# Kernel optimization log

Hardware: AMD Instinct MI355X
Metric: run time of the kernel (lower is better)

The kernel has to match this reference:

```python
import jax, jax.numpy as jnp
import numpy as np

N_NODES = 100000
N_EDGES = 1600000
FEAT = 128
HIDDEN = 128
NUM_CLASSES = 40


def setup_inputs() -> dict:
    key = jax.random.key(0)
    ks = jax.random.split(key, 6)
    x = jax.random.normal(ks[0], (N_NODES, FEAT), dtype=jnp.float32)
    edge_index = jax.random.randint(ks[1], (2, N_EDGES), 0, N_NODES, dtype=jnp.int64)
    # GCNConv layer-1 params (glorot-ish scale) and trailing Linear params
    W1 = jax.random.normal(ks[2], (FEAT, HIDDEN), dtype=jnp.float32) / np.sqrt(FEAT)
    b1 = jnp.zeros((HIDDEN,), dtype=jnp.float32)
    lin_W = jax.random.normal(ks[3], (HIDDEN, NUM_CLASSES), dtype=jnp.float32) / np.sqrt(HIDDEN)
    lin_b = jnp.zeros((NUM_CLASSES,), dtype=jnp.float32)
    return {"x": x, "edge_index": edge_index, "W1": W1, "b1": b1,
            "lin_W": lin_W, "lin_b": lin_b}


def _gcn_conv(x, edge_index, W, b):
    """PyG GCNConv: out = D^{-1/2}(A+I)D^{-1/2} (x W) + b."""
    n = x.shape[0]
    self_loops = jnp.arange(n, dtype=edge_index.dtype)
    row = jnp.concatenate([edge_index[0], self_loops])  # source nodes
    col = jnp.concatenate([edge_index[1], self_loops])  # destination nodes
    deg = jax.ops.segment_sum(jnp.ones_like(col, dtype=x.dtype), col, num_segments=n)
    deg_inv_sqrt = jnp.where(deg > 0, jax.lax.rsqrt(deg), 0.0)
    norm = deg_inv_sqrt[row] * deg_inv_sqrt[col]  # [E+N]
    h = x @ W                                      # [N, H]
    msg = norm[:, None] * h[row]                   # [E+N, H] gather
    out = jax.ops.segment_sum(msg, col, num_segments=n)  # scatter-add
    return out + b


def reference(x, edge_index, W1, b1, lin_W, lin_b):
    h = _gcn_conv(x, edge_index, W1, b1)
    h = jax.nn.relu(h)
    # F.dropout with training=False (eval) is the identity
    logits = h @ lin_W + lin_b
    return jax.nn.log_softmax(logits, axis=1)
```

## Files before the change

### kernel.cpp

```cpp
#include <hip/hip_runtime.h>
#include <hip/hip_fp16.h>
#include <math.h>

#define N_NODES 100000
#define N_EDGES 1600000
#define NBUCK   1563
#define NBUCK_P 1568
#define NB_HIST 256
#define NB_BIN  256
#define DCAP    1536

#define OFF_BTOT   0x1000u
#define OFF_HS     0x780000u
#define OFF_WT     0x2100000u
#define OFF_WLT    0x2110000u
#define OFF_GHIST  0x3980000u
#define OFF_GCHOFF 0x3B10000u
#define OFF_DUMP   0x3CA0000u

typedef _Float16 half8_t __attribute__((ext_vector_type(8)));
typedef float f32x2_t __attribute__((ext_vector_type(2)));
typedef float f32x4_t __attribute__((ext_vector_type(4)));
typedef float f32x16_t __attribute__((ext_vector_type(16)));

__global__ __launch_bounds__(256) void k_hist(const int* __restrict__ p32,
                                              int* __restrict__ G_hist,
                                              const float* __restrict__ W,
                                              __half* __restrict__ Wt,
                                              const float* __restrict__ linW,
                                              __half* __restrict__ WlT) {
  const int t = threadIdx.x;
  if (blockIdx.x == NB_HIST + 16) {
    __shared__ float buf[5120];
#pragma unroll
    for (int i = 0; i < 5; ++i) {
      int lin = i * 256 + t;
      ((float4*)buf)[lin] = ((const float4*)linW)[lin];
    }
    __syncthreads();
#pragma unroll
    for (int i = 0; i < 4; ++i) {
      int lin = i * 256 + t;
      int c = lin >> 4, kb = lin & 15;
      union { __half h[8]; int4 v; } u;
#pragma unroll
      for (int q = 0; q < 8; ++q)
        u.h[q] = (c < 40) ? __float2half(buf[(kb * 8 + q) * 40 + c])
                          : __float2half(0.f);
      *(int4*)&WlT[(size_t)c * 128 + kb * 8] = u.v;
    }
    return;
  }
  if (blockIdx.x >= NB_HIST) {
    __shared__ float buf1[1024];
    const int b = blockIdx.x - NB_HIST;
    float4 v = ((const float4*)(W + (size_t)b * 1024))[t];
    *(float4*)&buf1[t * 4] = v;
    __syncthreads();
    if (t < 128) {
      union { __half h[8]; int4 v; } u;
#pragma unroll
      for (int k = 0; k < 8; ++k) u.h[k] = __float2half(buf1[k * 128 + t]);
      *(int4*)&Wt[(size_t)t * 128 + b * 8] = u.v;
    }
    return;
  }
  __shared__ int hist[NBUCK];
  __shared__ int nz;
  if (t == 0) nz = 0;
  for (int i = t; i < NBUCK; i += 256) hist[i] = 0;
  __syncthreads();
  if (p32[2 * t + 1] != 0) atomicAdd(&nz, 1);
  __syncthreads();
  const int s = (nz == 0) ? 1 : 0;
  const int base = blockIdx.x * 6250;
  for (int i = 0; i < 25; ++i) {
    int e = base + i * 256 + t;
    if (e < base + 6250) {
      int c = p32[((size_t)(N_EDGES + e)) << s];
      atomicAdd(&hist[c >> 6], 1);
    }
  }
  __syncthreads();
  for (int i = t; i < NBUCK; i += 256) G_hist[blockIdx.x * NBUCK_P + i] = hist[i];
}

__global__ __launch_bounds__(256) void k_bucket_scan(const int* __restrict__ G_hist,
                                                     int* __restrict__ G_choff,
                                                     int* __restrict__ btot) {
  __shared__ int wsum[4];
  const int t = threadIdx.x;
  const int b = blockIdx.x;
  const int c = G_hist[t * NBUCK_P + b];
  int sv = c;
  const int lane = t & 63;
  for (int d = 1; d < 64; d <<= 1) {
    int a = __shfl_up(sv, d);
    if (lane >= d) sv += a;
  }
  if (lane == 63) wsum[t >> 6] = sv;
  __syncthreads();
  int o = 0;
  for (int w2 = 0; w2 < (t >> 6); ++w2) o += wsum[w2];
  G_choff[t * NBUCK_P + b] = o + sv - c;
  if (t == 255) btot[b] = o + sv;
}

__global__ __launch_bounds__(512) void k_bin(const int* __restrict__ p32,
                                             const int* __restrict__ G_choff,
                                             int* __restrict__ dump) {
  __shared__ int gb[NBUCK];
  __shared__ int cur[NBUCK];
  __shared__ int nz;
  const int t = threadIdx.x;
  const int blk = blockIdx.x;
  if (t == 0) nz = 0;
  for (int i = t; i < NBUCK; i += 512) {
    gb[i] = i * DCAP + G_choff[blk * NBUCK_P + i];
    cur[i] = 0;
  }
  __syncthreads();
  if (t < 256 && p32[2 * t + 1] != 0) atomicAdd(&nz, 1);
  __syncthreads();
  const int s = (nz == 0) ? 1 : 0;
  const int base = blk * 6250;
  for (int i = 0; i < 13; ++i) {
    int e = base + i * 512 + t;
    if (e < base + 6250) {
      int r = p32[((size_t)e) << s];
      int c = p32[((size_t)(N_EDGES + e)) << s];
      int bk = c >> 6;
      int p = atomicAdd(&cur[bk], 1);
      dump[gb[bk] + p] = (r << 6) | (c & 63);
    }
  }
}

__global__ __launch_bounds__(256, 3) void k_gemm1(
    const float* __restrict__ x, const __half* __restrict__ Wt,
    const int* __restrict__ dump, const int* __restrict__ btot,
    unsigned char* __restrict__ hs8) {
  __shared__ _Float16 xt[64 * 136];
  __shared__ _Float16 wt[128 * 136];
  __shared__ int c_s[64];
  const int t = threadIdx.x;
  const int b = blockIdx.x;
  const int row0 = b * 64;
  if (t < 64) c_s[t] = 0;
  __syncthreads();
#pragma unroll
  for (int i = 0; i < 8; ++i) {
    int lin = i * 256 + t;
    int r = lin >> 5, c4 = lin & 31;
    int gr = row0 + r;
    float4 v = make_float4(0.f, 0.f, 0.f, 0.f);
    if (gr < N_NODES) v = *(const float4*)(x + (size_t)gr * 128 + c4 * 4);
    union { __half2 h2[2]; int2 iv; } u;
    u.h2[0] = __floats2half2_rn(v.x, v.y);
    u.h2[1] = __floats2half2_rn(v.z, v.w);
    *(int2*)&xt[r * 136 + c4 * 4] = u.iv;
  }
#pragma unroll
  for (int i = 0; i < 8; ++i) {
    int lin = i * 256 + t;
    int n = lin >> 4, kb = lin & 15;
    int4 v = *(const int4*)(Wt + (size_t)n * 128 + kb * 8);
    *(int4*)&wt[n * 136 + kb * 8] = v;
  }
  {
    const int rb = b * DCAP;
    const int m = btot[b];
    for (int j = t; j < m; j += 256) atomicAdd(&c_s[dump[rb + j] & 63], 1);
  }
  __syncthreads();

  const int w = t >> 6, l = t & 63;
  const int r = l & 15, g = l >> 4;
  const _Float16* ap = &xt[(w * 16 + r) * 136 + g * 8];
  half8_t af[4];
#pragma unroll
  for (int ks = 0; ks < 4; ++ks) af[ks] = *(const half8_t*)&ap[ks * 32];

  const int lbase = w * 16 + g * 4;
  const int rbase = row0 + lbase;
  float dv[4];
#pragma unroll
  for (int j = 0; j < 4; ++j)
    dv[j] = rsqrtf((float)c_s[lbase + j] + 1.0f);

#pragma unroll
  for (int ct = 0; ct < 8; ++ct) {
    f32x4_t acc = {0.f, 0.f, 0.f, 0.f};
    const _Float16* bp = &wt[(ct * 16 + r) * 136 + g * 8];
#pragma unroll
    for (int ks = 0; ks < 4; ++ks) {
      half8_t bf = *(const half8_t*)&bp[ks * 32];
      acc = __builtin_amdgcn_mfma_f32_16x16x32_f16(af[ks], bf, acc, 0, 0, 0);
    }
#pragma unroll
    for (int j = 0; j < 4; ++j) {
      int rr = rbase + j;
      if (rr < N_NODES) {
        unsigned int pk =
            __builtin_amdgcn_cvt_pk_fp8_f32(acc[j] * dv[j], 0.f, 0u, false);
        hs8[(size_t)rr * 128 + ct * 16 + r] = (unsigned char)(pk & 0xffu);
      }
    }
  }
}

__global__ __launch_bounds__(512, 8) void k_aggfin(
    const unsigned char* __restrict__ hs8, const int* __restrict__ dump,
    const int* __restrict__ btot, const float* __restrict__ b1,
    const __half* __restrict__ WlT, const float* __restrict__ linb,
    float* __restrict__ out) {
  __shared__ int stage[4352];
  __shared__ _Float16 wlt[64 * 136];
  __shared__ float lb_s[64];
  __shared__ int cnt_s[64];
  __shared__ int off_s[64];
  __shared__ int cur_s[64];
  _Float16* vs = (_Float16*)stage;
  float* outbuf = (float*)stage;

  const int t = threadIdx.x;
  const int b = blockIdx.x;
  const int n0 = b << 6;
  if (t < 64) cnt_s[t] = 0;
#pragma unroll
  for (int i = 0; i < 2; ++i) {
    int lin = i * 512 + t;
    int c = lin >> 4, kb = lin & 15;
    int4 v = *(const int4*)(WlT + (size_t)c * 128 + kb * 8);
    *(int4*)&wlt[c * 136 + kb * 8] = v;
  }
  if (t < 64) lb_s[t] = (t < 40) ? linb[t] : 0.f;
  __syncthreads();

  const int rb = b * DCAP;
  const int m = btot[b];
  for (int j = t; j < m; j += 512) atomicAdd(&cnt_s[dump[rb + j] & 63], 1);
  __syncthreads();
  if (t < 64) {
    int v = cnt_s[t];
    int sv = v;
    for (int d = 1; d < 64; d <<= 1) {
      int u = __shfl_up(sv, d);
      if (t >= d) sv += u;
    }
    off_s[t] = sv - v;
    cur_s[t] = sv - v;
  }
  __syncthreads();
  for (int j = t; j < m; j += 512) {
    int rec = dump[rb + j];
    int p = atomicAdd(&cur_s[rec & 63], 1);
    stage[p] = rec >> 6;
  }
  __syncthreads();

  const int hw = t >> 5, lane = t & 31;
  uint2 res[4];
#pragma unroll
  for (int mi = 0; mi < 4; ++mi) {
    res[mi] = make_uint2(0u, 0u);
    const int i = hw + mi * 16;
    const int n = n0 + i;
    if (n >= N_NODES) continue;
    f32x4_t sum;
    {
      unsigned int raw = *(const unsigned int*)(hs8 + (size_t)n * 128 + lane * 4);
      f32x2_t lo = __builtin_amdgcn_cvt_pk_f32_fp8(raw, false);
      f32x2_t hi = __builtin_amdgcn_cvt_pk_f32_fp8(raw, true);
      sum[0] = lo[0]; sum[1] = lo[1]; sum[2] = hi[0]; sum[3] = hi[1];
    }
    int j = off_s[i];
    const int e0 = off_s[i] + cnt_s[i];
    for (; j + 8 <= e0; j += 8) {
      unsigned int r[8];
#pragma unroll
      for (int q = 0; q < 8; ++q) {
        int src = stage[j + q];
        r[q] = *(const unsigned int*)(hs8 + (size_t)src * 128 + lane * 4);
      }
#pragma unroll
      for (int q = 0; q < 8; ++q) {
        f32x2_t lo = __builtin_amdgcn_cvt_pk_f32_fp8(r[q], false);
        f32x2_t hi = __builtin_amdgcn_cvt_pk_f32_fp8(r[q], true);
        f32x4_t v; v[0] = lo[0]; v[1] = lo[1]; v[2] = hi[0]; v[3] = hi[1];
        sum += v;
      }
    }
    if (j + 4 <= e0) {
      unsigned int r[4];
#pragma unroll
      for (int q = 0; q < 4; ++q) {
        int src = stage[j + q];
        r[q] = *(const unsigned int*)(hs8 + (size_t)src * 128 + lane * 4);
      }
#pragma unroll
      for (int q = 0; q < 4; ++q) {
        f32x2_t lo = __builtin_amdgcn_cvt_pk_f32_fp8(r[q], false);
        f32x2_t hi = __builtin_amdgcn_cvt_pk_f32_fp8(r[q], true);
        f32x4_t v; v[0] = lo[0]; v[1] = lo[1]; v[2] = hi[0]; v[3] = hi[1];
        sum += v;
      }
      j += 4;
    }
    for (; j < e0; ++j) {
      int src = stage[j];
      unsigned int raw = *(const unsigned int*)(hs8 + (size_t)src * 128 + lane * 4);
      f32x2_t lo = __builtin_amdgcn_cvt_pk_f32_fp8(raw, false);
      f32x2_t hi = __builtin_amdgcn_cvt_pk_f32_fp8(raw, true);
      f32x4_t v; v[0] = lo[0]; v[1] = lo[1]; v[2] = hi[0]; v[3] = hi[1];
      sum += v;
    }
    float d = rsqrtf((float)cnt_s[i] + 1.0f);
    float4 bb = *(const float4*)(b1 + lane * 4);
    union { __half2 h[2]; uint2 v; } u;
    u.h[0] = __floats2half2_rn(fmaxf(fmaf(d, sum[0], bb.x), 0.f),
                               fmaxf(fmaf(d, sum[1], bb.y), 0.f));
    u.h[1] = __floats2half2_rn(fmaxf(fmaf(d, sum[2], bb.z), 0.f),
                               fmaxf(fmaf(d, sum[3], bb.w), 0.f));
    res[mi] = u.v;
  }
  __syncthreads();
#pragma unroll
  for (int mi = 0; mi < 4; ++mi) {
    const int i = hw + mi * 16;
    *(uint2*)&vs[i * 136 + lane * 4] = res[mi];
  }
  __syncthreads();

  const int wv = t >> 6, l64 = t & 63;
  f32x16_t C = {};
  int colg = 0, lbv_valid = 0;
  float lbv = 0.f;
  if (wv < 4) {
    const int rowt = wv >> 1, colt = wv & 1;
    const int rw = l64 & 31, kg = l64 >> 5;
    const _Float16* ap = &vs[(rowt * 32 + rw) * 136 + kg * 8];
    const _Float16* bp = &wlt[(colt * 32 + rw) * 136 + kg * 8];
#pragma unroll
    for (int ks = 0; ks < 8; ++ks) {
      half8_t af = *(const half8_t*)&ap[ks * 16];
      half8_t bf = *(const half8_t*)&bp[ks * 16];
      C = __builtin_amdgcn_mfma_f32_32x32x16_f16(af, bf, C, 0, 0, 0);
    }
    colg = colt * 32 + rw;
    lbv = lb_s[colg];
    lbv_valid = 1;
  }
  __syncthreads();
  if (lbv_valid && colg < 40) {
    const int rowt = (t >> 6) >> 1;
    const int hi = (t & 63) >> 5;
#pragma unroll
    for (int q = 0; q < 16; ++q) {
      int row = (q & 3) + 8 * (q >> 2) + 4 * hi;
      outbuf[(rowt * 32 + row) * 68 + colg] = C[q] + lbv;
    }
  }
  __syncthreads();

  const int node = t >> 3;
  const int cg = (t & 7) * 5;
  const int n = n0 + node;
  float lg[5];
#pragma unroll
  for (int j = 0; j < 5; ++j) lg[j] = outbuf[node * 68 + cg + j];
  float mx = lg[0];
#pragma unroll
  for (int j = 1; j < 5; ++j) mx = fmaxf(mx, lg[j]);
  mx = fmaxf(mx, __shfl_xor(mx, 1));
  mx = fmaxf(mx, __shfl_xor(mx, 2));
  mx = fmaxf(mx, __shfl_xor(mx, 4));
  float ssum = 0.f;
#pragma unroll
  for (int j = 0; j < 5; ++j) ssum += expf(lg[j] - mx);
  ssum += __shfl_xor(ssum, 1);
  ssum += __shfl_xor(ssum, 2);
  ssum += __shfl_xor(ssum, 4);
  float lse = mx + logf(ssum);
  if (n < N_NODES) {
#pragma unroll
    for (int j = 0; j < 5; ++j) out[(size_t)n * 40 + cg + j] = lg[j] - lse;
  }
}

extern "C" void kernel_launch(void* const* d_in, const int* in_sizes, int n_in,
                              void* d_out, int out_size, void* d_ws, size_t ws_size,
                              hipStream_t stream) {
  const float* x    = (const float*)d_in[0];
  const int*   ei   = (const int*)d_in[1];
  const float* W1   = (const float*)d_in[2];
  const float* b1   = (const float*)d_in[3];
  const float* linW = (const float*)d_in[4];
  const float* linb = (const float*)d_in[5];
  float* out = (float*)d_out;
  char* ws = (char*)d_ws;

  int*           btot   = (int*)(ws + OFF_BTOT);
  unsigned char* hs8    = (unsigned char*)(ws + OFF_HS);
  __half*        Wt     = (__half*)(ws + OFF_WT);
  __half*        WlT    = (__half*)(ws + OFF_WLT);
  int*           ghist  = (int*)(ws + OFF_GHIST);
  int*           gchoff = (int*)(ws + OFF_GCHOFF);
  int*           dump   = (int*)(ws + OFF_DUMP);

  k_hist<<<NB_HIST + 17, 256, 0, stream>>>(ei, ghist, W1, Wt, linW, WlT);
  k_bucket_scan<<<NBUCK, 256, 0, stream>>>(ghist, gchoff, btot);
  k_bin<<<NB_BIN, 512, 0, stream>>>(ei, gchoff, dump);
  k_gemm1<<<NBUCK, 256, 0, stream>>>(x, Wt, dump, btot, hs8);
  k_aggfin<<<NBUCK, 512, 0, stream>>>(hs8, dump, btot, b1, WlT, linb, out);
}
```

Measured before the change: 104.6 us.

## Drop LDS staging of weights and inputs, load fragments directly from global

The GEMM kernel now loads x rows and W fragments straight from global memory (through cache) into MFMA registers instead of staging them in shared memory. This cuts LDS use and raises the launch-bounds occupancy target. The aggregation/finalize kernel likewise reads the linear-layer weights directly from global and moves from 512 to 256 threads per block, with each thread handling more nodes and the softmax split across 4 lanes instead of 8. The goal is higher occupancy and less LDS traffic and synchronization, at the cost of redundant global/L2 weight reads and more work per thread.

```diff
diff --git a/kernel.cpp b/kernel.cpp
--- a/kernel.cpp
+++ b/kernel.cpp
@@ -136,50 +136,41 @@
   }
 }
 
-__global__ __launch_bounds__(256, 3) void k_gemm1(
+__global__ __launch_bounds__(256, 6) void k_gemm1(
     const float* __restrict__ x, const __half* __restrict__ Wt,
     const int* __restrict__ dump, const int* __restrict__ btot,
     unsigned char* __restrict__ hs8) {
-  __shared__ _Float16 xt[64 * 136];
-  __shared__ _Float16 wt[128 * 136];
   __shared__ int c_s[64];
   const int t = threadIdx.x;
   const int b = blockIdx.x;
   const int row0 = b * 64;
   if (t < 64) c_s[t] = 0;
   __syncthreads();
-#pragma unroll
-  for (int i = 0; i < 8; ++i) {
-    int lin = i * 256 + t;
-    int r = lin >> 5, c4 = lin & 31;
-    int gr = row0 + r;
-    float4 v = make_float4(0.f, 0.f, 0.f, 0.f);
-    if (gr < N_NODES) v = *(const float4*)(x + (size_t)gr * 128 + c4 * 4);
-    union { __half2 h2[2]; int2 iv; } u;
-    u.h2[0] = __floats2half2_rn(v.x, v.y);
-    u.h2[1] = __floats2half2_rn(v.z, v.w);
-    *(int2*)&xt[r * 136 + c4 * 4] = u.iv;
-  }
-#pragma unroll
-  for (int i = 0; i < 8; ++i) {
-    int lin = i * 256 + t;
-    int n = lin >> 4, kb = lin & 15;
-    int4 v = *(const int4*)(Wt + (size_t)n * 128 + kb * 8);
-    *(int4*)&wt[n * 136 + kb * 8] = v;
-  }
   {
     const int rb = b * DCAP;
     const int m = btot[b];
     for (int j = t; j < m; j += 256) atomicAdd(&c_s[dump[rb + j] & 63], 1);
   }
-  __syncthreads();
-
   const int w = t >> 6, l = t & 63;
   const int r = l & 15, g = l >> 4;
-  const _Float16* ap = &xt[(w * 16 + r) * 136 + g * 8];
+  const int arow = row0 + w * 16 + r;
   half8_t af[4];
 #pragma unroll
-  for (int ks = 0; ks < 4; ++ks) af[ks] = *(const half8_t*)&ap[ks * 32];
+  for (int ks = 0; ks < 4; ++ks) {
+    float4 v0 = make_float4(0.f, 0.f, 0.f, 0.f), v1 = v0;
+    if (arow < N_NODES) {
+      const float* xp = x + (size_t)arow * 128 + ks * 32 + g * 8;
+      v0 = *(const float4*)xp;
+      v1 = *(const float4*)(xp + 4);
+    }
+    half8_t h;
+    h[0] = (_Float16)v0.x; h[1] = (_Float16)v0.y;
+    h[2] = (_Float16)v0.z; h[3] = (_Float16)v0.w;
+    h[4] = (_Float16)v1.x; h[5] = (_Float16)v1.y;
+    h[6] = (_Float16)v1.z; h[7] = (_Float16)v1.w;
+    af[ks] = h;
+  }
+  __syncthreads();
 
   const int lbase = w * 16 + g * 4;
   const int rbase = row0 + lbase;
@@ -191,10 +182,10 @@
 #pragma unroll
   for (int ct = 0; ct < 8; ++ct) {
     f32x4_t acc = {0.f, 0.f, 0.f, 0.f};
-    const _Float16* bp = &wt[(ct * 16 + r) * 136 + g * 8];
+    const __half* bp = Wt + (size_t)(ct * 16 + r) * 128 + g * 8;
 #pragma unroll
     for (int ks = 0; ks < 4; ++ks) {
-      half8_t bf = *(const half8_t*)&bp[ks * 32];
+      half8_t bf = *(const half8_t*)(bp + ks * 32);
       acc = __builtin_amdgcn_mfma_f32_16x16x32_f16(af[ks], bf, acc, 0, 0, 0);
     }
 #pragma unroll
@@ -209,13 +200,12 @@
   }
 }
 
-__global__ __launch_bounds__(512, 8) void k_aggfin(
+__global__ __launch_bounds__(256, 6) void k_aggfin(
     const unsigned char* __restrict__ hs8, const int* __restrict__ dump,
     const int* __restrict__ btot, const float* __restrict__ b1,
     const __half* __restrict__ WlT, const float* __restrict__ linb,
     float* __restrict__ out) {
   __shared__ int stage[4352];
-  __shared__ _Float16 wlt[64 * 136];
   __shared__ float lb_s[64];
   __shared__ int cnt_s[64];
   __shared__ int off_s[64];
@@ -227,19 +217,12 @@
   const int b = blockIdx.x;
   const int n0 = b << 6;
   if (t < 64) cnt_s[t] = 0;
-#pragma unroll
-  for (int i = 0; i < 2; ++i) {
-    int lin = i * 512 + t;
-    int c = lin >> 4, kb = lin & 15;
-    int4 v = *(const int4*)(WlT + (size_t)c * 128 + kb * 8);
-    *(int4*)&wlt[c * 136 + kb * 8] = v;
-  }
-  if (t < 64) lb_s[t] = (t < 40) ? linb[t] : 0.f;
+  if (t >= 64 && t < 128) lb_s[t - 64] = (t - 64 < 40) ? linb[t - 64] : 0.f;
   __syncthreads();
 
   const int rb = b * DCAP;
   const int m = btot[b];
-  for (int j = t; j < m; j += 512) atomicAdd(&cnt_s[dump[rb + j] & 63], 1);
+  for (int j = t; j < m; j += 256) atomicAdd(&cnt_s[dump[rb + j] & 63], 1);
   __syncthreads();
   if (t < 64) {
     int v = cnt_s[t];
@@ -252,7 +235,7 @@
     cur_s[t] = sv - v;
   }
   __syncthreads();
-  for (int j = t; j < m; j += 512) {
+  for (int j = t; j < m; j += 256) {
     int rec = dump[rb + j];
     int p = atomicAdd(&cur_s[rec & 63], 1);
     stage[p] = rec >> 6;
@@ -260,11 +243,11 @@
   __syncthreads();
 
   const int hw = t >> 5, lane = t & 31;
-  uint2 res[4];
-#pragma unroll
-  for (int mi = 0; mi < 4; ++mi) {
+  uint2 res[8];
+#pragma unroll
+  for (int mi = 0; mi < 8; ++mi) {
     res[mi] = make_uint2(0u, 0u);
-    const int i = hw + mi * 16;
+    const int i = hw + mi * 8;
     const int n = n0 + i;
     if (n >= N_NODES) continue;
     f32x4_t sum;
@@ -326,35 +309,31 @@
   }
   __syncthreads();
 #pragma unroll
-  for (int mi = 0; mi < 4; ++mi) {
-    const int i = hw + mi * 16;
+  for (int mi = 0; mi < 8; ++mi) {
+    const int i = hw + mi * 8;
     *(uint2*)&vs[i * 136 + lane * 4] = res[mi];
   }
   __syncthreads();
 
   const int wv = t >> 6, l64 = t & 63;
+  const int rowt = wv >> 1, colt = wv & 1;
+  const int rw = l64 & 31, kg = l64 >> 5;
   f32x16_t C = {};
-  int colg = 0, lbv_valid = 0;
-  float lbv = 0.f;
-  if (wv < 4) {
-    const int rowt = wv >> 1, colt = wv & 1;
-    const int rw = l64 & 31, kg = l64 >> 5;
+  {
     const _Float16* ap = &vs[(rowt * 32 + rw) * 136 + kg * 8];
-    const _Float16* bp = &wlt[(colt * 32 + rw) * 136 + kg * 8];
+    const __half* bp = WlT + (size_t)(colt * 32 + rw) * 128 + kg * 8;
 #pragma unroll
     for (int ks = 0; ks < 8; ++ks) {
       half8_t af = *(const half8_t*)&ap[ks * 16];
-      half8_t bf = *(const half8_t*)&bp[ks * 16];
+      half8_t bf = *(const half8_t*)(bp + ks * 16);
       C = __builtin_amdgcn_mfma_f32_32x32x16_f16(af, bf, C, 0, 0, 0);
     }
-    colg = colt * 32 + rw;
-    lbv = lb_s[colg];
-    lbv_valid = 1;
-  }
-  __syncthreads();
-  if (lbv_valid && colg < 40) {
-    const int rowt = (t >> 6) >> 1;
-    const int hi = (t & 63) >> 5;
+  }
+  const int colg = colt * 32 + rw;
+  const float lbv = lb_s[colg];
+  __syncthreads();
+  if (colg < 40) {
+    const int hi = kg;
 #pragma unroll
     for (int q = 0; q < 16; ++q) {
       int row = (q & 3) + 8 * (q >> 2) + 4 * hi;
@@ -363,28 +342,26 @@
   }
   __syncthreads();
 
-  const int node = t >> 3;
-  const int cg = (t & 7) * 5;
+  const int node = t >> 2;
+  const int cg = (t & 3) * 10;
   const int n = n0 + node;
-  float lg[5];
-#pragma unroll
-  for (int j = 0; j < 5; ++j) lg[j] = outbuf[node * 68 + cg + j];
+  float lg[10];
+#pragma unroll
+  for (int j = 0; j < 10; ++j) lg[j] = outbuf[node * 68 + cg + j];
   float mx = lg[0];
 #pragma unroll
-  for (int j = 1; j < 5; ++j) mx = fmaxf(mx, lg[j]);
+  for (int j = 1; j < 10; ++j) mx = fmaxf(mx, lg[j]);
   mx = fmaxf(mx, __shfl_xor(mx, 1));
   mx = fmaxf(mx, __shfl_xor(mx, 2));
-  mx = fmaxf(mx, __shfl_xor(mx, 4));
   float ssum = 0.f;
 #pragma unroll
-  for (int j = 0; j < 5; ++j) ssum += expf(lg[j] - mx);
+  for (int j = 0; j < 10; ++j) ssum += expf(lg[j] - mx);
   ssum += __shfl_xor(ssum, 1);
   ssum += __shfl_xor(ssum, 2);
-  ssum += __shfl_xor(ssum, 4);
   float lse = mx + logf(ssum);
   if (n < N_NODES) {
 #pragma unroll
-    for (int j = 0; j < 5; ++j) out[(size_t)n * 40 + cg + j] = lg[j] - lse;
+    for (int j = 0; j < 10; ++j) out[(size_t)n * 40 + cg + j] = lg[j] - lse;
   }
 }
 
@@ -412,5 +389,5 @@
   k_bucket_scan<<<NBUCK, 256, 0, stream>>>(ghist, gchoff, btot);
   k_bin<<<NB_BIN, 512, 0, stream>>>(ei, gchoff, dump);
   k_gemm1<<<NBUCK, 256, 0, stream>>>(x, Wt, dump, btot, hs8);
-  k_aggfin<<<NBUCK, 512, 0, stream>>>(hs8, dump, btot, b1, WlT, linb, out);
-}
+  k_aggfin<<<NBUCK, 256, 0, stream>>>(hs8, dump, btot, b1, WlT, linb, out);
+}
```

Result: slower. 124.0 us (+18.6%).
